# Performance work log

Measured on AMD Instinct MI355X. Metric: run time of the kernel, lower is better.

## Reference

```python
import jax, jax.numpy as jnp
import numpy as np

B, L, D = 2, 256, 256


def setup_inputs() -> dict:
    key = jax.random.key(0)
    k1, k2, k3, k4 = jax.random.split(key, 4)
    x = jax.random.normal(k1, (B, L, D), dtype=jnp.float32)
    # nn.Linear(dim, 2*dim, bias=False): weight (2*dim, dim), out = x @ W.T
    W_a = jax.random.normal(k2, (2 * D, D), dtype=jnp.float32) / np.sqrt(D).astype(np.float32)
    # last_hidden_init: complex (dim,) parameter, split into real/imag floats
    h0_real = jax.random.normal(k3, (D,), dtype=jnp.float32)
    h0_imag = jax.random.normal(k4, (D,), dtype=jnp.float32)
    return {"x": x, "W_a": W_a, "h0_real": h0_real, "h0_imag": h0_imag}


def reference(x, W_a, h0_real, h0_imag):
    b, l, d = x.shape
    # a = view_as_complex(linear_a(x).float().view(b, l, d, 2))
    raw = (x.astype(jnp.float32) @ W_a.T).reshape(b, l, d, 2)
    re, im = raw[..., 0], raw[..., 1]
    mag2 = re * re + im * im                       # |a|^2
    a = jax.lax.complex(re, im) * (jax.lax.rsqrt(mag2) * jnp.exp(-mag2))
    a_ln = jnp.log(a)                              # (b, l, d) complex
    a_ln = jnp.transpose(a_ln, (0, 2, 1))          # (b, d, l)

    ii = jnp.arange(l)[:, None]
    kk = jnp.arange(l)[None, :]
    # a_ln_tri[b,d,i,k] = a_ln[b,d,k] if k >= i else 0 (== .triu())
    tri = jnp.where(kk >= ii, a_ln[:, :, None, :], 0.0)   # (b, d, l, l)
    # FFT causal conv with ones(len,len) row == cumulative sum along k
    cum = jnp.cumsum(tri, axis=-1)
    # c[b,d,i,k] = exp(sum_{j=i}^{k} a_ln_j) for k>=i, 1 at k=i-1, 0 below (.triu(-1))
    c = jnp.where(kk >= ii - 1, jnp.exp(cum), 0.0)         # (b, d, l, l)

    xT = jnp.transpose(x.astype(jnp.complex64), (0, 2, 1))  # (b, d, l)
    x_hat = jnp.roll(xT, 1, axis=2)                          # x_hat[k] = x[k-1]
    h0 = jax.lax.complex(h0_real, h0_imag)                   # (d,)
    x_hat = x_hat.at[:, :, 0].set(jnp.broadcast_to(h0, (b, d)))
    # x_mat does not depend on i, so (x_mat * c).sum(3) == einsum over k
    h = jnp.einsum('bdik,bdk->bdi', c, x_hat)
    h = h.at[:, :, -1].add(xT[:, :, -1])
    return jnp.transpose(h.real, (0, 2, 1)).astype(x.dtype)  # (b, l, d)
```

## Files before the change

kernel.cpp:

```cpp
#include <hip/hip_runtime.h>
#include <hip/hip_bf16.h>


constexpr int B = 2, L = 256, D = 256, K = 256;
constexpr int TL = 16;
constexpr int TD = 16;
constexpr int PAD = 260;

__global__ __launch_bounds__(256) void gemm_a_kernel(
    const float* __restrict__ x,
    const float* __restrict__ W,
    float2* __restrict__ a)
{
    const int dt = blockIdx.x;
    const int lt = blockIdx.y;
    const int b  = blockIdx.z;
    const int t  = threadIdx.x;
    const int l0 = lt * TL;
    const int d0 = dt * TD;
    const int r0 = 2 * d0;

    __shared__ float xs[TL][PAD];
    __shared__ float ws[2 * TD][PAD];

    {
        const float4* src = (const float4*)(x + (size_t)(b * L + l0) * K);
#pragma unroll
        for (int j = 0; j < 4; ++j) {
            const int g = j * 256 + t;
            const int row = g >> 6, c4 = g & 63;
            *(float4*)&xs[row][c4 * 4] = src[g];
        }
    }
    {
        const float4* src = (const float4*)(W + (size_t)r0 * K);
#pragma unroll
        for (int j = 0; j < 8; ++j) {
            const int g = j * 256 + t;
            const int row = g >> 6, c4 = g & 63;
            *(float4*)&ws[row][c4 * 4] = src[g];
        }
    }
    __syncthreads();

    const int l  = t >> 4;
    const int dd = t & 15;

    float re = 0.f, im = 0.f;
#pragma unroll 8
    for (int k4 = 0; k4 < K / 4; ++k4) {
        const float4 xv = *(const float4*)&xs[l][k4 * 4];
        const float4 w0 = *(const float4*)&ws[2 * dd][k4 * 4];
        const float4 w1 = *(const float4*)&ws[2 * dd + 1][k4 * 4];
        re += xv.x * w0.x + xv.y * w0.y + xv.z * w0.z + xv.w * w0.w;
        im += xv.x * w1.x + xv.y * w1.y + xv.z * w1.z + xv.w * w1.w;
    }

    const float m2 = re * re + im * im;
    const float s  = rsqrtf(m2) * expf(-m2);
    a[(size_t)(b * L + l0 + l) * D + d0 + dd] = make_float2(re * s, im * s);
}

__global__ __launch_bounds__(256) void scan_h_kernel(
    const float* __restrict__ x,
    const float2* __restrict__ a,
    const float* __restrict__ h0r,
    const float* __restrict__ h0i,
    float* __restrict__ out)
{
    const int b = blockIdx.x >> 8;
    const int d = blockIdx.x & 255;
    const int i = threadIdx.x;

    __shared__ float2 As[L];
    __shared__ float2 Bs[L];

    const size_t col = (size_t)b * L * D + d;

    const float2 ai = a[col + (size_t)i * D];
    float xr, xi;
    if (i == 0) { xr = h0r[d]; xi = h0i[d]; }
    else        { xr = x[col + (size_t)(i - 1) * D]; xi = 0.f; }

    float Ar = ai.x, Ai = ai.y;
    float Br = ai.x * xr - ai.y * xi;
    float Bi = ai.x * xi + ai.y * xr;

#pragma unroll
    for (int o = 1; o < L; o <<= 1) {
        As[i] = make_float2(Ar, Ai);
        Bs[i] = make_float2(Br, Bi);
        __syncthreads();
        if (i + o < L) {
            const float2 An = As[i + o];
            const float2 Bn = Bs[i + o];
            const float nAr = Ar * An.x - Ai * An.y;
            const float nAi = Ar * An.y + Ai * An.x;
            const float nBr = Ar * Bn.x - Ai * Bn.y + Br;
            const float nBi = Ar * Bn.y + Ai * Bn.x + Bi;
            Ar = nAr; Ai = nAi; Br = nBr; Bi = nBi;
        }
        __syncthreads();
    }

    float o_val = Br;
    if (i >= 2)      o_val += x[col + (size_t)(i - 2) * D];
    else if (i == 1) o_val += h0r[d];
    if (i == L - 1)  o_val += x[col + (size_t)(L - 1) * D];
    out[col + (size_t)i * D] = o_val;
}

extern "C" void kernel_launch(void* const* d_in, const int* in_sizes, int n_in,
                              void* d_out, int out_size, void* d_ws, size_t ws_size,
                              hipStream_t stream) {
    const float* x    = (const float*)d_in[0];
    const float* W_a  = (const float*)d_in[1];
    const float* h0r  = (const float*)d_in[2];
    const float* h0i  = (const float*)d_in[3];
    float* out = (float*)d_out;
    float2* a  = (float2*)d_ws;

    gemm_a_kernel<<<dim3(D / TD, L / TL, B), dim3(256), 0, stream>>>(x, W_a, a);
    scan_h_kernel<<<dim3(B * D), dim3(256), 0, stream>>>(x, a, h0r, h0i, out);
}
```

Measured before the change: 71.87 us.

## Transpose a layout, register-tile GEMM, swizzle W smem, cache x column in scan

Measured after the change: 69.25 us, median of 2. -3.6%, faster.

```diff
diff --git a/kernel.cpp b/kernel.cpp
--- a/kernel.cpp
+++ b/kernel.cpp
@@ -3,14 +3,14 @@
 
 
 constexpr int B = 2, L = 256, D = 256, K = 256;
-constexpr int TL = 16;
+constexpr int TL = 32;
 constexpr int TD = 16;
-constexpr int PAD = 260;
+constexpr int PADW = 260;
 
 __global__ __launch_bounds__(256) void gemm_a_kernel(
     const float* __restrict__ x,
     const float* __restrict__ W,
-    float2* __restrict__ a)
+    float2* __restrict__ aT)
 {
     const int dt = blockIdx.x;
     const int lt = blockIdx.y;
@@ -18,52 +18,61 @@
     const int t  = threadIdx.x;
     const int l0 = lt * TL;
     const int d0 = dt * TD;
-    const int r0 = 2 * d0;
 
-    __shared__ float xs[TL][PAD];
-    __shared__ float ws[2 * TD][PAD];
+    __shared__ float xs[TL][PADW];
+    __shared__ float ws[2 * TD][PADW];
 
     {
         const float4* src = (const float4*)(x + (size_t)(b * L + l0) * K);
 #pragma unroll
-        for (int j = 0; j < 4; ++j) {
+        for (int j = 0; j < 8; ++j) {
             const int g = j * 256 + t;
             const int row = g >> 6, c4 = g & 63;
             *(float4*)&xs[row][c4 * 4] = src[g];
         }
     }
     {
-        const float4* src = (const float4*)(W + (size_t)r0 * K);
+        const float4* src = (const float4*)(W + (size_t)(2 * d0) * K);
 #pragma unroll
         for (int j = 0; j < 8; ++j) {
             const int g = j * 256 + t;
             const int row = g >> 6, c4 = g & 63;
-            *(float4*)&ws[row][c4 * 4] = src[g];
+            *(float4*)&ws[row][(c4 ^ ((row >> 1) & 7)) * 4] = src[g];
         }
     }
     __syncthreads();
 
-    const int l  = t >> 4;
-    const int dd = t & 15;
+    const int dgrp = t & 15;
+    const int lgrp = t >> 4;
+    const int sw   = dgrp & 7;
 
-    float re = 0.f, im = 0.f;
+    float rr0 = 0.f, ii0 = 0.f, rr1 = 0.f, ii1 = 0.f;
 #pragma unroll 8
     for (int k4 = 0; k4 < K / 4; ++k4) {
-        const float4 xv = *(const float4*)&xs[l][k4 * 4];
-        const float4 w0 = *(const float4*)&ws[2 * dd][k4 * 4];
-        const float4 w1 = *(const float4*)&ws[2 * dd + 1][k4 * 4];
-        re += xv.x * w0.x + xv.y * w0.y + xv.z * w0.z + xv.w * w0.w;
-        im += xv.x * w1.x + xv.y * w1.y + xv.z * w1.z + xv.w * w1.w;
+        const int kc = (k4 ^ sw) * 4;
+        const float4 w0  = *(const float4*)&ws[2 * dgrp][kc];
+        const float4 w1  = *(const float4*)&ws[2 * dgrp + 1][kc];
+        const float4 xv0 = *(const float4*)&xs[2 * lgrp][k4 * 4];
+        const float4 xv1 = *(const float4*)&xs[2 * lgrp + 1][k4 * 4];
+        rr0 += xv0.x * w0.x + xv0.y * w0.y + xv0.z * w0.z + xv0.w * w0.w;
+        ii0 += xv0.x * w1.x + xv0.y * w1.y + xv0.z * w1.z + xv0.w * w1.w;
+        rr1 += xv1.x * w0.x + xv1.y * w0.y + xv1.z * w0.z + xv1.w * w0.w;
+        ii1 += xv1.x * w1.x + xv1.y * w1.y + xv1.z * w1.z + xv1.w * w1.w;
     }
 
-    const float m2 = re * re + im * im;
-    const float s  = rsqrtf(m2) * expf(-m2);
-    a[(size_t)(b * L + l0 + l) * D + d0 + dd] = make_float2(re * s, im * s);
+    const int d = d0 + dgrp;
+#pragma unroll
+    for (int i = 0; i < 2; ++i) {
+        const float re = i ? rr1 : rr0, im = i ? ii1 : ii0;
+        const float m2 = re * re + im * im;
+        const float s  = rsqrtf(m2) * expf(-m2);
+        aT[((size_t)b * D + d) * L + (l0 + 2 * lgrp + i)] = make_float2(re * s, im * s);
+    }
 }
 
 __global__ __launch_bounds__(256) void scan_h_kernel(
     const float* __restrict__ x,
-    const float2* __restrict__ a,
+    const float2* __restrict__ aT,
     const float* __restrict__ h0r,
     const float* __restrict__ h0i,
     float* __restrict__ out)
@@ -72,15 +81,18 @@
     const int d = blockIdx.x & 255;
     const int i = threadIdx.x;
 
-    __shared__ float2 As[L];
-    __shared__ float2 Bs[L];
+    __shared__ float4 Ms[L];
+    __shared__ float  xcol[L];
 
-    const size_t col = (size_t)b * L * D + d;
+    const size_t colbase = (size_t)b * L * D + d;
 
-    const float2 ai = a[col + (size_t)i * D];
+    const float2 ai = aT[((size_t)b * D + d) * L + i];
+    xcol[i] = x[colbase + (size_t)i * D];
+    __syncthreads();
+
     float xr, xi;
     if (i == 0) { xr = h0r[d]; xi = h0i[d]; }
-    else        { xr = x[col + (size_t)(i - 1) * D]; xi = 0.f; }
+    else        { xr = xcol[i - 1]; xi = 0.f; }
 
     float Ar = ai.x, Ai = ai.y;
     float Br = ai.x * xr - ai.y * xi;
@@ -88,26 +100,24 @@
 
 #pragma unroll
     for (int o = 1; o < L; o <<= 1) {
-        As[i] = make_float2(Ar, Ai);
-        Bs[i] = make_float2(Br, Bi);
+        Ms[i] = make_float4(Ar, Ai, Br, Bi);
         __syncthreads();
         if (i + o < L) {
-            const float2 An = As[i + o];
-            const float2 Bn = Bs[i + o];
-            const float nAr = Ar * An.x - Ai * An.y;
-            const float nAi = Ar * An.y + Ai * An.x;
-            const float nBr = Ar * Bn.x - Ai * Bn.y + Br;
-            const float nBi = Ar * Bn.y + Ai * Bn.x + Bi;
+            const float4 n = Ms[i + o];
+            const float nAr = Ar * n.x - Ai * n.y;
+            const float nAi = Ar * n.y + Ai * n.x;
+            const float nBr = Ar * n.z - Ai * n.w + Br;
+            const float nBi = Ar * n.w + Ai * n.z + Bi;
             Ar = nAr; Ai = nAi; Br = nBr; Bi = nBi;
         }
         __syncthreads();
     }
 
     float o_val = Br;
-    if (i >= 2)      o_val += x[col + (size_t)(i - 2) * D];
+    if (i >= 2)      o_val += xcol[i - 2];
     else if (i == 1) o_val += h0r[d];
-    if (i == L - 1)  o_val += x[col + (size_t)(L - 1) * D];
-    out[col + (size_t)i * D] = o_val;
+    if (i == L - 1)  o_val += xcol[L - 1];
+    out[colbase + (size_t)i * D] = o_val;
 }
 
 extern "C" void kernel_launch(void* const* d_in, const int* in_sizes, int n_in,
@@ -118,8 +128,8 @@
     const float* h0r  = (const float*)d_in[2];
     const float* h0i  = (const float*)d_in[3];
     float* out = (float*)d_out;
-    float2* a  = (float2*)d_ws;
+    float2* aT = (float2*)d_ws;
 
-    gemm_a_kernel<<<dim3(D / TD, L / TL, B), dim3(256), 0, stream>>>(x, W_a, a);
-    scan_h_kernel<<<dim3(B * D), dim3(256), 0, stream>>>(x, a, h0r, h0i, out);
+    gemm_a_kernel<<<dim3(D / TD, L / TL, B), dim3(256), 0, stream>>>(x, W_a, aT);
+    scan_h_kernel<<<dim3(B * D), dim3(256), 0, stream>>>(x, aT, h0r, h0i, out);
 }
```
